# Kernel tuning notes

Hardware: AMD Instinct MI355X
Metric: run time of the kernel (lower is better)

The kernel has to match this reference:

```python
import jax, jax.numpy as jnp
from jax import lax
import numpy as np
import math

EPSILON = 0.05
ITER = 50
HALF_SIZE = 1
K = 2 * HALF_SIZE + 1          # 3
SIZE = K * K                   # 9, matches (2*half_size+1)**2
LOG_SIZE = math.log(SIZE)


def _smooth_trans(x, ker):
    # exp -> replicate pad -> 3x3 box-sum conv -> log -> scale (soft max-pool / dilation)
    e = jnp.exp(x / EPSILON)
    e = jnp.pad(e, ((0, 0), (0, 0), (1, 1), (1, 1)), mode='edge')
    s = lax.conv_general_dilated(
        e, ker, window_strides=(1, 1), padding='VALID',
        dimension_numbers=('NCHW', 'OIHW', 'NCHW'))
    return EPSILON * (jnp.log(s) - LOG_SIZE)


def setup_inputs() -> dict:
    key = jax.random.key(0)
    img = jax.random.uniform(key, (8, 1, 512, 512), dtype=jnp.float32)
    ker = jnp.ones((1, 1, K, K), dtype=jnp.float32)
    return {"img": img, "ker": ker}


def reference(img, ker):
    def erode(x):
        return -_smooth_trans(-x, ker)

    def dilate(x):
        return _smooth_trans(x, ker)

    def open_(x):
        return jnp.clip(dilate(erode(x)), 0.0, 1.0)

    skel = jax.nn.relu(img - open_(img))

    def step(carry, _):
        im, sk = carry
        im = erode(im)
        sk = sk + jax.nn.relu(im - open_(im))
        return (im, sk), None

    (_, skel), _ = lax.scan(step, (img, skel), None, length=ITER)
    return skel
```

## Files before the change

### kernel.cpp

```cpp
#include <hip/hip_runtime.h>

#define HH 512
#define WW 512
#define NB 8
#define TH 32
#define TW 64
#define ST 80
#define RB 48
#define RO 8
#define CO 8

__device__ __forceinline__ float rcp_f(float x)  { return __builtin_amdgcn_rcpf(x); }
__device__ __forceinline__ float log2_f(float x) { return __builtin_amdgcn_logf(x); }
__device__ __forceinline__ float exp2_f(float x) { return __builtin_amdgcn_exp2f(x); }

#define C1      0.034657359027997264f
#define LOG2_9  3.1699250014423126f
#define NEG_INV -28.853900817779268f

__device__ __forceinline__ float4 ld4(const float* p) { return *(const float4*)p; }
__device__ __forceinline__ void   st4(float* p, float4 v) { *(float4*)p = v; }

template<int B_, bool LAST, bool E_IMG, bool WRITEU>
__device__ __forceinline__ void one_step(
    float* __restrict__ P, float* __restrict__ Q,
    int r0, int c0, int tid, bool edge,
    float* __restrict__ uog, const float* __restrict__ imgb,
    float4 (&sk)[2])
{
    constexpr int BC0 = (B_ == 5) ? 0 : 4;
    constexpr int BCL = ((71 + B_) >> 2) << 2;
    constexpr int NG  = (BCL - BC0) / 4 + 1;
    constexpr int RA0 = RO - 1 - B_;
    constexpr int NRA = TH + 2 + 2 * B_;
    constexpr int RB0 = RO - B_;
    constexpr int NRB = TH + 2 * B_;

    float4 e[2];
    if constexpr (!E_IMG) {
        #pragma unroll
        for (int j = 0; j < 2; ++j) {
            int gi = j * 256 + tid;
            int tr = RO + (gi >> 4), bc = CO + (gi & 15) * 4;
            float4 u = ld4(P + tr * ST + bc);
            e[j].x = -C1 * log2_f(u.x); e[j].y = -C1 * log2_f(u.y);
            e[j].z = -C1 * log2_f(u.z); e[j].w = -C1 * log2_f(u.w);
        }
    }

    for (int gi = tid; gi < NRA * NG; gi += 256) {
        int rr = gi / NG;
        int bc = BC0 + (gi - rr * NG) * 4;
        const float* row = P + (RA0 + rr) * ST;
        float4 q = ld4(row + bc);
        float pm1 = row[bc > 0 ? bc - 1 : 0];
        float p4  = row[bc + 4];
        float4 o;
        o.x = pm1 + q.x + q.y; o.y = q.x + q.y + q.z;
        o.z = q.y + q.z + q.w; o.w = q.z + q.w + p4;
        st4(Q + (RA0 + rr) * ST + bc, o);
    }
    __syncthreads();

    if (!edge) {
        for (int gi = tid; gi < NRB * NG; gi += 256) {
            int rr = gi / NG;
            int bc = BC0 + (gi - rr * NG) * 4;
            int r = RB0 + rr;
            const float* h = Q + (r - 1) * ST + bc;
            float4 t = ld4(h), m = ld4(h + ST), b = ld4(h + 2 * ST);
            float4 u;
            u.x = (t.x + m.x + b.x) * (1.0f / 9.0f);
            u.y = (t.y + m.y + b.y) * (1.0f / 9.0f);
            u.z = (t.z + m.z + b.z) * (1.0f / 9.0f);
            u.w = (t.w + m.w + b.w) * (1.0f / 9.0f);
            st4(P + r * ST + bc, u);
            if constexpr (LAST && WRITEU) {
                if (r >= RO && r < RO + TH && bc >= CO && bc < CO + TW)
                    *(float4*)(uog + (size_t)(r0 + r - RO) * WW + (c0 + bc - CO)) = u;
            }
        }
    } else {
        constexpr int WID = TW + 2 * B_;
        for (int i = tid; i < NRB * WID; i += 256) {
            int rr = i / WID;
            int c  = (CO - B_) + (i - rr * WID);
            int r  = RB0 + rr;
            int gr = r0 + r - RO, gc = c0 + c - CO;
            int rcl = min(max(gr, 0), HH - 1) - r0 + RO;
            int ccl = min(max(gc, 0), WW - 1) - c0 + CO;
            float u = (Q[(rcl - 1) * ST + ccl] + Q[rcl * ST + ccl] + Q[(rcl + 1) * ST + ccl]) * (1.0f / 9.0f);
            P[r * ST + c] = u;
            if constexpr (LAST && WRITEU) {
                if (r >= RO && r < RO + TH && c >= CO && c < CO + TW)
                    uog[(size_t)gr * WW + gc] = u;
            }
        }
    }
    __syncthreads();

    for (int gi = tid; gi < (TH + 2) * 16; gi += 256) {
        int rr = gi >> 4;
        int bc = CO + (gi & 15) * 4;
        const float* row = P + (RO - 1 + rr) * ST;
        float4 q = ld4(row + bc);
        float pm1 = row[bc - 1], p4 = row[bc + 4];
        float a0 = rcp_f(pm1), a1 = rcp_f(q.x), a2 = rcp_f(q.y),
              a3 = rcp_f(q.z), a4 = rcp_f(q.w), a5 = rcp_f(p4);
        float4 o;
        o.x = a0 + a1 + a2; o.y = a1 + a2 + a3;
        o.z = a2 + a3 + a4; o.w = a3 + a4 + a5;
        st4(Q + (RO - 1 + rr) * ST + bc, o);
    }
    __syncthreads();

    #pragma unroll
    for (int j = 0; j < 2; ++j) {
        int gi = j * 256 + tid;
        int tr = RO + (gi >> 4), bc = CO + (gi & 15) * 4;
        const float* h = Q + (tr - 1) * ST + bc;
        float4 t = ld4(h), m = ld4(h + ST), b = ld4(h + 2 * ST);
        float4 d;
        d.x = fminf(fmaxf(C1 * (log2_f(t.x + m.x + b.x) - LOG2_9), 0.0f), 1.0f);
        d.y = fminf(fmaxf(C1 * (log2_f(t.y + m.y + b.y) - LOG2_9), 0.0f), 1.0f);
        d.z = fminf(fmaxf(C1 * (log2_f(t.z + m.z + b.z) - LOG2_9), 0.0f), 1.0f);
        d.w = fminf(fmaxf(C1 * (log2_f(t.w + m.w + b.w) - LOG2_9), 0.0f), 1.0f);
        float4 ee;
        if constexpr (E_IMG)
            ee = *(const float4*)(imgb + (size_t)(r0 + tr - RO) * WW + (c0 + bc - CO));
        else
            ee = e[j];
        sk[j].x += fmaxf(ee.x - d.x, 0.0f);
        sk[j].y += fmaxf(ee.y - d.y, 0.0f);
        sk[j].z += fmaxf(ee.z - d.z, 0.0f);
        sk[j].w += fmaxf(ee.w - d.w, 0.0f);
    }
    __syncthreads();
}

template<int B_, int REMAIN, bool E_IMG, bool WRITEU>
struct Chain {
    static __device__ __forceinline__ void run(
        float* P, float* Q, int r0, int c0, int tid, bool edge,
        float* uog, const float* imgb, float4 (&sk)[2])
    {
        one_step<B_, (REMAIN == 1), E_IMG, WRITEU>(P, Q, r0, c0, tid, edge, uog, imgb, sk);
        if constexpr (REMAIN > 1)
            Chain<B_ - 1, REMAIN - 1, false, WRITEU>::run(P, Q, r0, c0, tid, edge, uog, imgb, sk);
    }
};

template<bool FIRST, int NSTEP, bool WRITEU>
__global__ __launch_bounds__(256)
void sk_fused(const float* __restrict__ u_in, const float* __restrict__ img,
              float* __restrict__ u_out, float* __restrict__ skel)
{
    constexpr int A0 = NSTEP + 1;
    __shared__ __align__(16) float P[RB * ST];
    __shared__ __align__(16) float Q[RB * ST];

    const int r0  = blockIdx.y * TH;
    const int c0  = blockIdx.x * TW;
    const int tid = threadIdx.x;
    const bool edge = (blockIdx.x == 0) | (blockIdx.x == gridDim.x - 1) |
                      (blockIdx.y == 0) | (blockIdx.y == gridDim.y - 1);
    const size_t boff = (size_t)blockIdx.z * (HH * WW);
    const float* imgb = img + boff;
    float* uog = u_out + boff;
    float* skb = skel + boff;

    {
        constexpr int SH = TH + 2 * A0, SW = TW + 2 * A0;
        const float* uin = u_in + boff;
        for (int i = tid; i < SH * SW; i += 256) {
            int rr = i / SW, cc = i - rr * SW;
            int gr = min(max(r0 + rr - A0, 0), HH - 1);
            int gc = min(max(c0 + cc - A0, 0), WW - 1);
            float v;
            if constexpr (FIRST) v = exp2_f(imgb[gr * WW + gc] * NEG_INV);
            else                 v = uin[gr * WW + gc];
            P[(RO - A0 + rr) * ST + (CO - A0 + cc)] = v;
        }
    }
    __syncthreads();

    float4 sk[2];
    sk[0] = make_float4(0.f, 0.f, 0.f, 0.f);
    sk[1] = make_float4(0.f, 0.f, 0.f, 0.f);

    Chain<NSTEP, NSTEP, FIRST, WRITEU>::run(P, Q, r0, c0, tid, edge, uog, imgb, sk);

    #pragma unroll
    for (int j = 0; j < 2; ++j) {
        int gi = j * 256 + tid;
        int tr = RO + (gi >> 4), bc = CO + (gi & 15) * 4;
        float* sp = skb + (size_t)(r0 + tr - RO) * WW + (c0 + bc - CO);
        if constexpr (FIRST) {
            *(float4*)sp = sk[j];
        } else {
            float4 old = *(const float4*)sp;
            old.x += sk[j].x; old.y += sk[j].y; old.z += sk[j].z; old.w += sk[j].w;
            *(float4*)sp = old;
        }
    }
}

extern "C" void kernel_launch(void* const* d_in, const int* in_sizes, int n_in,
                              void* d_out, int out_size, void* d_ws, size_t ws_size,
                              hipStream_t stream) {
    const float* img = (const float*)d_in[0];
    float* skel = (float*)d_out;
    const size_t N = (size_t)NB * HH * WW;
    float* ua = (float*)d_ws;
    float* ub = ua + N;

    dim3 grid(WW / TW, HH / TH, NB);

    sk_fused<true, 5, true><<<grid, 256, 0, stream>>>(nullptr, img, ua, skel);

    float* uin = ua; float* uout = ub;
    for (int t = 0; t < 9; ++t) {
        sk_fused<false, 5, true><<<grid, 256, 0, stream>>>(uin, img, uout, skel);
        float* tmp = uin; uin = uout; uout = tmp;
    }

    sk_fused<false, 1, false><<<grid, 256, 0, stream>>>(uin, img, uout, skel);
}
```

Before: 443.6 us.

## Fuse separable stencil passes into single-pass 3x3 with ping-pong LDS buffers

Replaces the separate horizontal and vertical box-sum passes, each followed by a barrier, with one direct 3x3 pass. The two LDS buffers now swap roles between steps. The reciprocal horizontal pass is folded into the final dilation stage, and the erode value is recomputed from the input buffer instead of being kept in registers. This removes two barriers and one LDS round trip per step, at the cost of more LDS reads and redundant reciprocal and add work per output.

```diff
diff --git a/kernel.cpp b/kernel.cpp
--- a/kernel.cpp
+++ b/kernel.cpp
@@ -20,97 +20,59 @@
 
 __device__ __forceinline__ float4 ld4(const float* p) { return *(const float4*)p; }
 __device__ __forceinline__ void   st4(float* p, float4 v) { *(float4*)p = v; }
+__device__ __forceinline__ float clamp01(float x) { return fminf(fmaxf(x, 0.0f), 1.0f); }
 
 template<int B_, bool LAST, bool E_IMG, bool WRITEU>
 __device__ __forceinline__ void one_step(
-    float* __restrict__ P, float* __restrict__ Q,
+    const float* __restrict__ IN, float* __restrict__ OUT,
     int r0, int c0, int tid, bool edge,
-    float* __restrict__ uog, const float* __restrict__ imgb,
-    float4 (&sk)[2])
+    float* __restrict__ uog, const float* __restrict__ imgb, float4 (&sk)[2])
 {
-    constexpr int BC0 = (B_ == 5) ? 0 : 4;
-    constexpr int BCL = ((71 + B_) >> 2) << 2;
-    constexpr int NG  = (BCL - BC0) / 4 + 1;
-    constexpr int RA0 = RO - 1 - B_;
-    constexpr int NRA = TH + 2 + 2 * B_;
+    constexpr int BC0 = ((8 - B_) >> 2) << 2;
+    constexpr int LG  = ((71 + B_) >> 2) << 2;
+    constexpr int NG  = (LG - BC0) / 4 + 1;
     constexpr int RB0 = RO - B_;
     constexpr int NRB = TH + 2 * B_;
 
-    float4 e[2];
-    if constexpr (!E_IMG) {
-        #pragma unroll
-        for (int j = 0; j < 2; ++j) {
-            int gi = j * 256 + tid;
-            int tr = RO + (gi >> 4), bc = CO + (gi & 15) * 4;
-            float4 u = ld4(P + tr * ST + bc);
-            e[j].x = -C1 * log2_f(u.x); e[j].y = -C1 * log2_f(u.y);
-            e[j].z = -C1 * log2_f(u.z); e[j].w = -C1 * log2_f(u.w);
-        }
-    }
-
-    for (int gi = tid; gi < NRA * NG; gi += 256) {
+    for (int gi = tid; gi < NRB * NG; gi += 256) {
         int rr = gi / NG;
         int bc = BC0 + (gi - rr * NG) * 4;
-        const float* row = P + (RA0 + rr) * ST;
-        float4 q = ld4(row + bc);
-        float pm1 = row[bc > 0 ? bc - 1 : 0];
-        float p4  = row[bc + 4];
-        float4 o;
-        o.x = pm1 + q.x + q.y; o.y = q.x + q.y + q.z;
-        o.z = q.y + q.z + q.w; o.w = q.z + q.w + p4;
-        st4(Q + (RA0 + rr) * ST + bc, o);
-    }
-    __syncthreads();
-
-    if (!edge) {
-        for (int gi = tid; gi < NRB * NG; gi += 256) {
-            int rr = gi / NG;
-            int bc = BC0 + (gi - rr * NG) * 4;
-            int r = RB0 + rr;
-            const float* h = Q + (r - 1) * ST + bc;
-            float4 t = ld4(h), m = ld4(h + ST), b = ld4(h + 2 * ST);
+        int r  = RB0 + rr;
+        int gr = r0 + r - RO, gc0 = c0 + bc - CO;
+        bool vec = !edge || ((unsigned)gr < HH && (unsigned)gc0 <= (WW - 4));
+        if (vec) {
+            const float* p0 = IN + (r - 1) * ST;
+            const float* p1 = IN + r * ST;
+            const float* p2 = IN + (r + 1) * ST;
+            float4 a = ld4(p0 + bc), b = ld4(p1 + bc), c4 = ld4(p2 + bc);
+            float  m = p0[bc - 1] + p1[bc - 1] + p2[bc - 1];
+            float  p = p0[bc + 4] + p1[bc + 4] + p2[bc + 4];
+            float4 cv;
+            cv.x = a.x + b.x + c4.x; cv.y = a.y + b.y + c4.y;
+            cv.z = a.z + b.z + c4.z; cv.w = a.w + b.w + c4.w;
             float4 u;
-            u.x = (t.x + m.x + b.x) * (1.0f / 9.0f);
-            u.y = (t.y + m.y + b.y) * (1.0f / 9.0f);
-            u.z = (t.z + m.z + b.z) * (1.0f / 9.0f);
-            u.w = (t.w + m.w + b.w) * (1.0f / 9.0f);
-            st4(P + r * ST + bc, u);
+            u.x = (m    + cv.x + cv.y) * (1.0f / 9.0f);
+            u.y = (cv.x + cv.y + cv.z) * (1.0f / 9.0f);
+            u.z = (cv.y + cv.z + cv.w) * (1.0f / 9.0f);
+            u.w = (cv.z + cv.w + p)    * (1.0f / 9.0f);
+            st4(OUT + r * ST + bc, u);
             if constexpr (LAST && WRITEU) {
                 if (r >= RO && r < RO + TH && bc >= CO && bc < CO + TW)
-                    *(float4*)(uog + (size_t)(r0 + r - RO) * WW + (c0 + bc - CO)) = u;
+                    st4(uog + (size_t)gr * WW + gc0, u);
             }
-        }
-    } else {
-        constexpr int WID = TW + 2 * B_;
-        for (int i = tid; i < NRB * WID; i += 256) {
-            int rr = i / WID;
-            int c  = (CO - B_) + (i - rr * WID);
-            int r  = RB0 + rr;
-            int gr = r0 + r - RO, gc = c0 + c - CO;
+        } else {
             int rcl = min(max(gr, 0), HH - 1) - r0 + RO;
-            int ccl = min(max(gc, 0), WW - 1) - c0 + CO;
-            float u = (Q[(rcl - 1) * ST + ccl] + Q[rcl * ST + ccl] + Q[(rcl + 1) * ST + ccl]) * (1.0f / 9.0f);
-            P[r * ST + c] = u;
-            if constexpr (LAST && WRITEU) {
-                if (r >= RO && r < RO + TH && c >= CO && c < CO + TW)
-                    uog[(size_t)gr * WW + gc] = u;
+            #pragma unroll
+            for (int k = 0; k < 4; ++k) {
+                int gc = gc0 + k;
+                int ccl = min(max(gc, 0), WW - 1) - c0 + CO;
+                const float* q = IN + (rcl - 1) * ST + ccl;
+                float u = (q[-1] + q[0] + q[1] +
+                           q[ST - 1] + q[ST] + q[ST + 1] +
+                           q[2 * ST - 1] + q[2 * ST] + q[2 * ST + 1]) * (1.0f / 9.0f);
+                OUT[r * ST + bc + k] = u;
             }
         }
-    }
-    __syncthreads();
-
-    for (int gi = tid; gi < (TH + 2) * 16; gi += 256) {
-        int rr = gi >> 4;
-        int bc = CO + (gi & 15) * 4;
-        const float* row = P + (RO - 1 + rr) * ST;
-        float4 q = ld4(row + bc);
-        float pm1 = row[bc - 1], p4 = row[bc + 4];
-        float a0 = rcp_f(pm1), a1 = rcp_f(q.x), a2 = rcp_f(q.y),
-              a3 = rcp_f(q.z), a4 = rcp_f(q.w), a5 = rcp_f(p4);
-        float4 o;
-        o.x = a0 + a1 + a2; o.y = a1 + a2 + a3;
-        o.z = a2 + a3 + a4; o.w = a3 + a4 + a5;
-        st4(Q + (RO - 1 + rr) * ST + bc, o);
     }
     __syncthreads();
 
@@ -118,18 +80,30 @@
     for (int j = 0; j < 2; ++j) {
         int gi = j * 256 + tid;
         int tr = RO + (gi >> 4), bc = CO + (gi & 15) * 4;
-        const float* h = Q + (tr - 1) * ST + bc;
-        float4 t = ld4(h), m = ld4(h + ST), b = ld4(h + 2 * ST);
+        const float* q0 = OUT + (tr - 1) * ST;
+        const float* q1 = OUT + tr * ST;
+        const float* q2 = OUT + (tr + 1) * ST;
+        float4 a = ld4(q0 + bc), b = ld4(q1 + bc), c4 = ld4(q2 + bc);
+        float4 vs;
+        vs.x = rcp_f(a.x) + rcp_f(b.x) + rcp_f(c4.x);
+        vs.y = rcp_f(a.y) + rcp_f(b.y) + rcp_f(c4.y);
+        vs.z = rcp_f(a.z) + rcp_f(b.z) + rcp_f(c4.z);
+        vs.w = rcp_f(a.w) + rcp_f(b.w) + rcp_f(c4.w);
+        float vm = rcp_f(q0[bc - 1]) + rcp_f(q1[bc - 1]) + rcp_f(q2[bc - 1]);
+        float vp = rcp_f(q0[bc + 4]) + rcp_f(q1[bc + 4]) + rcp_f(q2[bc + 4]);
         float4 d;
-        d.x = fminf(fmaxf(C1 * (log2_f(t.x + m.x + b.x) - LOG2_9), 0.0f), 1.0f);
-        d.y = fminf(fmaxf(C1 * (log2_f(t.y + m.y + b.y) - LOG2_9), 0.0f), 1.0f);
-        d.z = fminf(fmaxf(C1 * (log2_f(t.z + m.z + b.z) - LOG2_9), 0.0f), 1.0f);
-        d.w = fminf(fmaxf(C1 * (log2_f(t.w + m.w + b.w) - LOG2_9), 0.0f), 1.0f);
+        d.x = clamp01(C1 * (log2_f(vm   + vs.x + vs.y) - LOG2_9));
+        d.y = clamp01(C1 * (log2_f(vs.x + vs.y + vs.z) - LOG2_9));
+        d.z = clamp01(C1 * (log2_f(vs.y + vs.z + vs.w) - LOG2_9));
+        d.w = clamp01(C1 * (log2_f(vs.z + vs.w + vp)   - LOG2_9));
         float4 ee;
-        if constexpr (E_IMG)
-            ee = *(const float4*)(imgb + (size_t)(r0 + tr - RO) * WW + (c0 + bc - CO));
-        else
-            ee = e[j];
+        if constexpr (E_IMG) {
+            ee = ld4(imgb + (size_t)(r0 + tr - RO) * WW + (c0 + bc - CO));
+        } else {
+            float4 u = ld4(IN + tr * ST + bc);
+            ee.x = -C1 * log2_f(u.x); ee.y = -C1 * log2_f(u.y);
+            ee.z = -C1 * log2_f(u.z); ee.w = -C1 * log2_f(u.w);
+        }
         sk[j].x += fmaxf(ee.x - d.x, 0.0f);
         sk[j].y += fmaxf(ee.y - d.y, 0.0f);
         sk[j].z += fmaxf(ee.z - d.z, 0.0f);
@@ -141,12 +115,12 @@
 template<int B_, int REMAIN, bool E_IMG, bool WRITEU>
 struct Chain {
     static __device__ __forceinline__ void run(
-        float* P, float* Q, int r0, int c0, int tid, bool edge,
+        float* IN, float* OUT, int r0, int c0, int tid, bool edge,
         float* uog, const float* imgb, float4 (&sk)[2])
     {
-        one_step<B_, (REMAIN == 1), E_IMG, WRITEU>(P, Q, r0, c0, tid, edge, uog, imgb, sk);
+        one_step<B_, (REMAIN == 1), E_IMG, WRITEU>(IN, OUT, r0, c0, tid, edge, uog, imgb, sk);
         if constexpr (REMAIN > 1)
-            Chain<B_ - 1, REMAIN - 1, false, WRITEU>::run(P, Q, r0, c0, tid, edge, uog, imgb, sk);
+            Chain<B_ - 1, REMAIN - 1, false, WRITEU>::run(OUT, IN, r0, c0, tid, edge, uog, imgb, sk);
     }
 };
 
```

After: 625.4 us. 41.0% more time.

## Fuse seven erosion steps per launch and vectorize edge-tile separable pass

Applied to the files above, without the earlier changes.

Raises the temporal fusion depth from five to seven steps per kernel launch, cutting the launch count and the global round-trips of the intermediate field, at the cost of wider halos and more redundant recomputation per tile. The shared-memory row stride grows to fit the wider halo and the column start is generalised for the larger radius. The edge-tile vertical pass is merged into the vectorized loop, falling back to a scalar clamped path only for groups that touch image borders, instead of running a fully scalar loop for all border blocks.

```diff
diff --git a/kernel.cpp b/kernel.cpp
--- a/kernel.cpp
+++ b/kernel.cpp
@@ -5,7 +5,7 @@
 #define NB 8
 #define TH 32
 #define TW 64
-#define ST 80
+#define ST 84
 #define RB 48
 #define RO 8
 #define CO 8
@@ -20,6 +20,7 @@
 
 __device__ __forceinline__ float4 ld4(const float* p) { return *(const float4*)p; }
 __device__ __forceinline__ void   st4(float* p, float4 v) { *(float4*)p = v; }
+__device__ __forceinline__ float clamp01(float x) { return fminf(fmaxf(x, 0.0f), 1.0f); }
 
 template<int B_, bool LAST, bool E_IMG, bool WRITEU>
 __device__ __forceinline__ void one_step(
@@ -28,7 +29,7 @@
     float* __restrict__ uog, const float* __restrict__ imgb,
     float4 (&sk)[2])
 {
-    constexpr int BC0 = (B_ == 5) ? 0 : 4;
+    constexpr int BC0 = ((8 - B_) >> 2) << 2;
     constexpr int BCL = ((71 + B_) >> 2) << 2;
     constexpr int NG  = (BCL - BC0) / 4 + 1;
     constexpr int RA0 = RO - 1 - B_;
@@ -62,11 +63,13 @@
     }
     __syncthreads();
 
-    if (!edge) {
-        for (int gi = tid; gi < NRB * NG; gi += 256) {
-            int rr = gi / NG;
-            int bc = BC0 + (gi - rr * NG) * 4;
-            int r = RB0 + rr;
+    for (int gi = tid; gi < NRB * NG; gi += 256) {
+        int rr = gi / NG;
+        int bc = BC0 + (gi - rr * NG) * 4;
+        int r  = RB0 + rr;
+        int gr = r0 + r - RO, gc0 = c0 + bc - CO;
+        bool vec = !edge || ((unsigned)gr < HH && (unsigned)gc0 <= (WW - 4));
+        if (vec) {
             const float* h = Q + (r - 1) * ST + bc;
             float4 t = ld4(h), m = ld4(h + ST), b = ld4(h + 2 * ST);
             float4 u;
@@ -77,23 +80,17 @@
             st4(P + r * ST + bc, u);
             if constexpr (LAST && WRITEU) {
                 if (r >= RO && r < RO + TH && bc >= CO && bc < CO + TW)
-                    *(float4*)(uog + (size_t)(r0 + r - RO) * WW + (c0 + bc - CO)) = u;
+                    st4(uog + (size_t)gr * WW + gc0, u);
             }
-        }
-    } else {
-        constexpr int WID = TW + 2 * B_;
-        for (int i = tid; i < NRB * WID; i += 256) {
-            int rr = i / WID;
-            int c  = (CO - B_) + (i - rr * WID);
-            int r  = RB0 + rr;
-            int gr = r0 + r - RO, gc = c0 + c - CO;
-            int rcl = min(max(gr, 0), HH - 1) - r0 + RO;
-            int ccl = min(max(gc, 0), WW - 1) - c0 + CO;
-            float u = (Q[(rcl - 1) * ST + ccl] + Q[rcl * ST + ccl] + Q[(rcl + 1) * ST + ccl]) * (1.0f / 9.0f);
-            P[r * ST + c] = u;
-            if constexpr (LAST && WRITEU) {
-                if (r >= RO && r < RO + TH && c >= CO && c < CO + TW)
-                    uog[(size_t)gr * WW + gc] = u;
+        } else {
+            #pragma unroll
+            for (int k = 0; k < 4; ++k) {
+                int gc = gc0 + k;
+                int rcl = min(max(gr, 0), HH - 1) - r0 + RO;
+                int ccl = min(max(gc, 0), WW - 1) - c0 + CO;
+                float u = (Q[(rcl - 1) * ST + ccl] + Q[rcl * ST + ccl] +
+                           Q[(rcl + 1) * ST + ccl]) * (1.0f / 9.0f);
+                P[r * ST + bc + k] = u;
             }
         }
     }
@@ -121,13 +118,13 @@
         const float* h = Q + (tr - 1) * ST + bc;
         float4 t = ld4(h), m = ld4(h + ST), b = ld4(h + 2 * ST);
         float4 d;
-        d.x = fminf(fmaxf(C1 * (log2_f(t.x + m.x + b.x) - LOG2_9), 0.0f), 1.0f);
-        d.y = fminf(fmaxf(C1 * (log2_f(t.y + m.y + b.y) - LOG2_9), 0.0f), 1.0f);
-        d.z = fminf(fmaxf(C1 * (log2_f(t.z + m.z + b.z) - LOG2_9), 0.0f), 1.0f);
-        d.w = fminf(fmaxf(C1 * (log2_f(t.w + m.w + b.w) - LOG2_9), 0.0f), 1.0f);
+        d.x = clamp01(C1 * (log2_f(t.x + m.x + b.x) - LOG2_9));
+        d.y = clamp01(C1 * (log2_f(t.y + m.y + b.y) - LOG2_9));
+        d.z = clamp01(C1 * (log2_f(t.z + m.z + b.z) - LOG2_9));
+        d.w = clamp01(C1 * (log2_f(t.w + m.w + b.w) - LOG2_9));
         float4 ee;
         if constexpr (E_IMG)
-            ee = *(const float4*)(imgb + (size_t)(r0 + tr - RO) * WW + (c0 + bc - CO));
+            ee = ld4(imgb + (size_t)(r0 + tr - RO) * WW + (c0 + bc - CO));
         else
             ee = e[j];
         sk[j].x += fmaxf(ee.x - d.x, 0.0f);
@@ -216,13 +213,13 @@
 
     dim3 grid(WW / TW, HH / TH, NB);
 
-    sk_fused<true, 5, true><<<grid, 256, 0, stream>>>(nullptr, img, ua, skel);
+    sk_fused<true, 7, true><<<grid, 256, 0, stream>>>(nullptr, img, ua, skel);
 
     float* uin = ua; float* uout = ub;
-    for (int t = 0; t < 9; ++t) {
-        sk_fused<false, 5, true><<<grid, 256, 0, stream>>>(uin, img, uout, skel);
+    for (int t = 0; t < 6; ++t) {
+        sk_fused<false, 7, true><<<grid, 256, 0, stream>>>(uin, img, uout, skel);
         float* tmp = uin; uin = uout; uout = tmp;
     }
 
-    sk_fused<false, 1, false><<<grid, 256, 0, stream>>>(uin, img, uout, skel);
+    sk_fused<false, 2, false><<<grid, 256, 0, stream>>>(uin, img, uout, skel);
 }
```

Result: no change. 444.2 us (+0.1%).
